# Optimization experiments

Measured on AMD Instinct MI355X. Metric: run time of the kernel, lower is better.

Reference implementation:

```python
import jax, jax.numpy as jnp
import numpy as np

IN_CH = 12      # InChannels global in original code
GROWTH = 12     # growth global == growthRate
H = 34          # peptide/pseudo-sequence length (long==34 branch)
BN_EPS = 1e-5


def setup_inputs() -> dict:
    key = jax.random.key(0)
    k = jax.random.split(key, 5)
    B, C = 16384, 72  # C = IN_CH + 5*GROWTH
    x = jax.random.normal(k[0], (B, C, H, 1), dtype=jnp.float32)
    gamma = jnp.ones((C,), dtype=jnp.float32)
    beta = jnp.zeros((C,), dtype=jnp.float32)
    conv_w = jax.random.normal(k[1], (GROWTH, C, 3, 1), dtype=jnp.float32) * 0.05
    fc_w = jax.random.normal(k[2], (1, H), dtype=jnp.float32)
    fc_bias = jax.random.normal(k[3], (1,), dtype=jnp.float32)
    return {"x": x, "gamma": gamma, "beta": beta, "conv_w": conv_w,
            "fc_w": fc_w, "fc_bias": fc_bias}


def reference(x, gamma, beta, conv_w, fc_w, fc_bias):
    B, C, Hh, Ww = x.shape
    n = (C - IN_CH) // GROWTH  # number of growth groups
    sg = jax.lax.stop_gradient

    x1 = x[:, :IN_CH]                                 # [B,12,H,1]
    x2g = x[:, IN_CH:].reshape(B, n, GROWTH, Hh, 1)    # [B,n,g,H,1]

    # per-group channel means, squeezed over the width-1 axis -> [B,n,H]
    m = x2g.mean(axis=2)[..., 0]
    x11 = x1.mean(axis=1)[..., 0]                      # [B,H]

    w = fc_w[0]                                        # [H]
    lin_m = m @ w + fc_bias[0]                         # [B,n]  (bias included per F.linear call)
    lin_out = lin_m[:, -1]                             # lin(x_outt), [B]
    lin_x11 = x11 @ w + fc_bias[0]                     # [B]

    # gate for x1: sigmoid(lin(x_outt) + lin(x11)); note bias appears twice, as in torch
    g1 = jax.nn.sigmoid(lin_out + lin_x11)             # [B]
    # gates for groups 0..n-2: sigmoid(lin(group_i) + lin(x_outt))
    gates = jax.nn.sigmoid(lin_m[:, :-1] + lin_out[:, None])  # [B,n-1]

    # the expand/repeat/view dance collapses to a per-sample scalar gate broadcast
    x1g = g1[:, None, None, None] * sg(x1)             # x1 is detached in original
    # groups are appended in reversed order (i = n-2 .. 0)
    gg = gates[:, ::-1][:, :, None, None, None] * sg(x2g[:, :-1][:, ::-1])
    gg_flat = gg.reshape(B, (n - 1) * GROWTH, Hh, 1)
    x_out = x2g[:, -1]                                 # last group, appended ungated

    xxx = jnp.concatenate([x1g, gg_flat, x_out], axis=1)  # [B,C,H,1]

    # BatchNorm2d in training mode (batch statistics, biased variance)
    mu = xxx.mean(axis=(0, 2, 3), keepdims=True)
    var = xxx.var(axis=(0, 2, 3), keepdims=True)
    xn = (xxx - mu) * jax.lax.rsqrt(var + BN_EPS)
    h = jax.nn.relu(gamma[None, :, None, None] * xn + beta[None, :, None, None])

    # Conv2d(C -> GROWTH, kernel (3,1), padding (1,0), no bias)
    out = jax.lax.conv_general_dilated(
        h, conv_w, window_strides=(1, 1), padding=((1, 1), (0, 0)),
        dimension_numbers=("NCHW", "OIHW", "NCHW"))

    return jnp.concatenate([x, out], axis=1)           # [B, C+GROWTH, H, 1]
```

## Files before the change

kernel.cpp:

```cpp
#include <hip/hip_runtime.h>
#include <math.h>


#define BN_EPS 1e-5f

#define WS_S    0
#define WS_SS   72
#define WS_A    144
#define WS_B    216
#define WS_WT   288
#define WS_GATE (288 + 3456)

__device__ __forceinline__ float sigmoidf_(float z) { return 1.f / (1.f + expf(-z)); }

__global__ __launch_bounds__(256) void k1_stats(const float* __restrict__ x,
                                                const float* __restrict__ fw,
                                                const float* __restrict__ fb,
                                                float* __restrict__ ws,
                                                int B, int nTrip)
{
    __shared__ float xs[3 * 2520];
    __shared__ float rs_s[3][72];
    __shared__ float rss_s[3][72];
    __shared__ float wsum_s[3][72];
    __shared__ float sc_s[3][8];
    __shared__ float Sacc[72], SSacc[72];

    const int tid = threadIdx.x;
    if (tid < 72) { Sacc[tid] = 0.f; SSacc[tid] = 0.f; }

    for (int t = blockIdx.x; t < nTrip; t += gridDim.x) {
        const int b0 = t * 3;

        for (int idx = tid; idx < 3 * 612; idx += 256) {
            int g = idx / 612, v = idx - g * 612;
            int b = b0 + g;
            if (b < B) {
                float4 q = ((const float4*)(x + (size_t)b * 2448))[v];
                float vv[4] = {q.x, q.y, q.z, q.w};
#pragma unroll
                for (int j = 0; j < 4; ++j) {
                    int e = v * 4 + j;
                    int c = e / 34, h = e - c * 34;
                    xs[g * 2520 + c * 35 + h] = vv[j];
                }
            }
        }
        __syncthreads();

        if (tid < 216) {
            int g = tid / 72, c = tid - g * 72;
            float rs = 0.f, rss = 0.f, wsm = 0.f;
            if (b0 + g < B) {
                const float* p = &xs[g * 2520 + c * 35];
#pragma unroll
                for (int h = 0; h < 34; ++h) {
                    float v = p[h];
                    rs += v;
                    rss = fmaf(v, v, rss);
                    wsm = fmaf(v, fw[h], wsm);
                }
            }
            rs_s[g][c] = rs; rss_s[g][c] = rss; wsum_s[g][c] = wsm;
        }
        __syncthreads();

        if (tid < 3 && b0 + tid < B) {
            int g = tid;
            float lm[6];
#pragma unroll
            for (int r = 0; r < 6; ++r) {
                float s = 0.f;
                for (int c = 0; c < 12; ++c) s += wsum_s[g][r * 12 + c];
                lm[r] = s * (1.f / 12.f) + fb[0];
            }
            float lin_out = lm[5];
            float sc[6];
            sc[0] = sigmoidf_(lin_out + lm[0]);
            sc[1] = sigmoidf_(lm[4] + lin_out);
            sc[2] = sigmoidf_(lm[3] + lin_out);
            sc[3] = sigmoidf_(lm[2] + lin_out);
            sc[4] = sigmoidf_(lm[1] + lin_out);
            sc[5] = 1.f;
            float* gb = ws + WS_GATE + (size_t)(b0 + g) * 6;
#pragma unroll
            for (int r = 0; r < 6; ++r) { sc_s[g][r] = sc[r]; gb[r] = sc[r]; }
        }
        __syncthreads();

        if (tid < 72) {
            const int c = tid;
            const int r = c / 12;
            const int dd[6] = {0, 36, 12, -12, -36, 0};
            const int src = c + dd[r];
            float a = 0.f, q = 0.f;
#pragma unroll
            for (int g = 0; g < 3; ++g) {
                if (b0 + g < B) {
                    float s = sc_s[g][r];
                    a = fmaf(s, rs_s[g][src], a);
                    q = fmaf(s * s, rss_s[g][src], q);
                }
            }
            Sacc[c] += a; SSacc[c] += q;
        }
        __syncthreads();
    }

    if (tid < 72) {
        atomicAdd(&ws[WS_S + tid], Sacc[tid]);
        atomicAdd(&ws[WS_SS + tid], SSacc[tid]);
    }
}

__global__ void k2_finalize(const float* __restrict__ gamma,
                            const float* __restrict__ beta,
                            const float* __restrict__ cw,
                            float* __restrict__ ws, float invN)
{
    const int tid = threadIdx.x;
    if (tid < 72) {
        float S = ws[WS_S + tid], SS = ws[WS_SS + tid];
        float mu = S * invN;
        float var = SS * invN - mu * mu;
        float inv = rsqrtf(var + BN_EPS);
        float A = gamma[tid] * inv;
        ws[WS_A + tid] = A;
        ws[WS_B + tid] = beta[tid] - mu * A;
    }
    for (int i = tid; i < 12 * 72 * 3; i += 256) {
        int o = i / 216, rem = i - o * 216;
        int c = rem / 3, k = rem - c * 3;
        ws[WS_WT + c * 48 + o * 4 + k] = cw[i];
    }
}

__global__ __launch_bounds__(256) void k3_out(const float* __restrict__ x,
                                              const float* __restrict__ ws,
                                              float* __restrict__ out, int B)
{
    __shared__ float hp[6 * 2592];
    __shared__ float2 AB[72];
    __shared__ float gl[6][8];

    const int tid = threadIdx.x;
    const int b0 = blockIdx.x * 6;
    int nb = B - b0; if (nb > 6) nb = 6;

    if (tid < 72) AB[tid] = make_float2(ws[WS_A + tid], ws[WS_B + tid]);
    for (int t2 = tid; t2 < nb * 6; t2 += 256) {
        int g = t2 / 6, j = t2 - g * 6;
        gl[g][j] = ws[WS_GATE + (size_t)(b0 + g) * 6 + j];
    }
    for (int t2 = tid; t2 < nb * 72; t2 += 256) {
        int g = t2 / 72, c = t2 - g * 72;
        hp[g * 2592 + c * 36] = 0.f;
        hp[g * 2592 + c * 36 + 35] = 0.f;
    }
    __syncthreads();

    for (int idx = tid; idx < nb * 612; idx += 256) {
        int g = idx / 612, v = idx - g * 612;
        size_t b = (size_t)(b0 + g);
        float4 q = ((const float4*)(x + b * 2448))[v];
        ((float4*)(out + b * 2856))[v] = q;
        float vv[4] = {q.x, q.y, q.z, q.w};
#pragma unroll
        for (int j = 0; j < 4; ++j) {
            int e = v * 4 + j;
            int cx = e / 34, h = e - cx * 34;
            const int ddv[6]  = {0, 36, 12, -12, -36, 0};
            const int sidx[6] = {0, 4, 3, 2, 1, 5};
            int rx = cx / 12;
            int cdst = cx + ddv[rx];
            float2 ab = AB[cdst];
            float s = gl[g][sidx[rx]];
            hp[g * 2592 + cdst * 36 + h + 1] = fmaxf(fmaf(ab.x * s, vv[j], ab.y), 0.f);
        }
    }
    __syncthreads();

    const float4* wT = (const float4*)(ws + WS_WT);
    for (int it = tid; it < nb * 34; it += 256) {
        int g = it / 34, hh = it - g * 34;
        const float* hb = &hp[g * 2592];
        float acc[12];
#pragma unroll
        for (int o = 0; o < 12; ++o) acc[o] = 0.f;
        for (int c = 0; c < 72; ++c) {
            float h0 = hb[c * 36 + hh];
            float h1 = hb[c * 36 + hh + 1];
            float h2 = hb[c * 36 + hh + 2];
#pragma unroll
            for (int o = 0; o < 12; ++o) {
                float4 wv = wT[c * 12 + o];
                acc[o] = fmaf(h0, wv.x, fmaf(h1, wv.y, fmaf(h2, wv.z, acc[o])));
            }
        }
        float* op = out + (size_t)(b0 + g) * 2856 + 2448;
#pragma unroll
        for (int o = 0; o < 12; ++o) op[o * 34 + hh] = acc[o];
    }
}

extern "C" void kernel_launch(void* const* d_in, const int* in_sizes, int n_in,
                              void* d_out, int out_size, void* d_ws, size_t ws_size,
                              hipStream_t stream)
{
    const float* x     = (const float*)d_in[0];
    const float* gamma = (const float*)d_in[1];
    const float* beta  = (const float*)d_in[2];
    const float* cw    = (const float*)d_in[3];
    const float* fw    = (const float*)d_in[4];
    const float* fb    = (const float*)d_in[5];
    float* out = (float*)d_out;
    float* ws  = (float*)d_ws;

    const int B = in_sizes[0] / (72 * 34);
    const int nTrip = (B + 2) / 3;

    hipMemsetAsync(ws, 0, 144 * sizeof(float), stream);

    k1_stats<<<1024, 256, 0, stream>>>(x, fw, fb, ws, B, nTrip);
    k2_finalize<<<1, 256, 0, stream>>>(gamma, beta, cw, ws, 1.f / ((float)B * 34.f));
    const int nb3 = (B + 5) / 6;
    k3_out<<<nb3, 256, 0, stream>>>(x, ws, out, B);
}
```

Measured before the change: 470.0 us.

## Read stats directly from global, store activations in fp16 LDS, deterministic partial reduce

```diff
diff --git a/kernel.cpp b/kernel.cpp
--- a/kernel.cpp
+++ b/kernel.cpp
@@ -1,4 +1,5 @@
 #include <hip/hip_runtime.h>
+#include <hip/hip_fp16.h>
 #include <math.h>
 
 
@@ -9,7 +10,8 @@
 #define WS_A    144
 #define WS_B    216
 #define WS_WT   288
-#define WS_GATE (288 + 3456)
+#define WS_GATE 3744
+#define K1_BLOCKS 512
 
 __device__ __forceinline__ float sigmoidf_(float z) { return 1.f / (1.f + expf(-z)); }
 
@@ -17,106 +19,100 @@
                                                 const float* __restrict__ fw,
                                                 const float* __restrict__ fb,
                                                 float* __restrict__ ws,
+                                                float* __restrict__ part,
                                                 int B, int nTrip)
 {
-    __shared__ float xs[3 * 2520];
-    __shared__ float rs_s[3][72];
-    __shared__ float rss_s[3][72];
-    __shared__ float wsum_s[3][72];
+    __shared__ float rs_s[3][72], rss_s[3][72], wsum_s[3][72];
+    __shared__ float lm_s[3][6];
     __shared__ float sc_s[3][8];
-    __shared__ float Sacc[72], SSacc[72];
+    __shared__ float Sacc[144];
 
     const int tid = threadIdx.x;
-    if (tid < 72) { Sacc[tid] = 0.f; SSacc[tid] = 0.f; }
-
-    for (int t = blockIdx.x; t < nTrip; t += gridDim.x) {
+    const int g = tid / 72;
+    const int c = tid - g * 72;
+    if (tid < 144) Sacc[tid] = 0.f;
+
+    for (int t = blockIdx.x; t < nTrip; t += K1_BLOCKS) {
         const int b0 = t * 3;
 
-        for (int idx = tid; idx < 3 * 612; idx += 256) {
-            int g = idx / 612, v = idx - g * 612;
-            int b = b0 + g;
-            if (b < B) {
-                float4 q = ((const float4*)(x + (size_t)b * 2448))[v];
-                float vv[4] = {q.x, q.y, q.z, q.w};
-#pragma unroll
-                for (int j = 0; j < 4; ++j) {
-                    int e = v * 4 + j;
-                    int c = e / 34, h = e - c * 34;
-                    xs[g * 2520 + c * 35 + h] = vv[j];
+        if (tid < 216 && b0 + g < B) {
+            const float2* p = (const float2*)(x + (size_t)(b0 + g) * 2448 + c * 34);
+            float rs = 0.f, rss = 0.f, wsm = 0.f;
+#pragma unroll
+            for (int i = 0; i < 17; ++i) {
+                float2 v = p[i];
+                rs += v.x + v.y;
+                rss = fmaf(v.x, v.x, fmaf(v.y, v.y, rss));
+                wsm = fmaf(v.x, fw[2 * i], fmaf(v.y, fw[2 * i + 1], wsm));
+            }
+            rs_s[g][c] = rs; rss_s[g][c] = rss; wsum_s[g][c] = wsm;
+        }
+        __syncthreads();
+
+        if (tid < 18) {
+            int gg = tid / 6, r = tid - gg * 6;
+            float s = 0.f;
+#pragma unroll
+            for (int k = 0; k < 12; ++k) s += wsum_s[gg][r * 12 + k];
+            lm_s[gg][r] = s * (1.f / 12.f) + fb[0];
+        }
+        __syncthreads();
+
+        if (tid < 3 && b0 + tid < B) {
+            float lin_out = lm_s[tid][5];
+            float sc[6];
+            sc[0] = sigmoidf_(lin_out + lm_s[tid][0]);
+            sc[1] = sigmoidf_(lm_s[tid][4] + lin_out);
+            sc[2] = sigmoidf_(lm_s[tid][3] + lin_out);
+            sc[3] = sigmoidf_(lm_s[tid][2] + lin_out);
+            sc[4] = sigmoidf_(lm_s[tid][1] + lin_out);
+            sc[5] = 1.f;
+            float* gb = ws + WS_GATE + (size_t)(b0 + tid) * 6;
+#pragma unroll
+            for (int r = 0; r < 6; ++r) { sc_s[tid][r] = sc[r]; gb[r] = sc[r]; }
+        }
+        __syncthreads();
+
+        if (tid < 72) {
+            const int r = tid / 12;
+            const int dd[6] = {0, 36, 12, -12, -36, 0};
+            const int src = tid + dd[r];
+            float a = 0.f, q = 0.f;
+#pragma unroll
+            for (int gg = 0; gg < 3; ++gg) {
+                if (b0 + gg < B) {
+                    float s = sc_s[gg][r];
+                    a = fmaf(s, rs_s[gg][src], a);
+                    q = fmaf(s * s, rss_s[gg][src], q);
                 }
             }
-        }
-        __syncthreads();
-
-        if (tid < 216) {
-            int g = tid / 72, c = tid - g * 72;
-            float rs = 0.f, rss = 0.f, wsm = 0.f;
-            if (b0 + g < B) {
-                const float* p = &xs[g * 2520 + c * 35];
-#pragma unroll
-                for (int h = 0; h < 34; ++h) {
-                    float v = p[h];
-                    rs += v;
-                    rss = fmaf(v, v, rss);
-                    wsm = fmaf(v, fw[h], wsm);
-                }
-            }
-            rs_s[g][c] = rs; rss_s[g][c] = rss; wsum_s[g][c] = wsm;
-        }
-        __syncthreads();
-
-        if (tid < 3 && b0 + tid < B) {
-            int g = tid;
-            float lm[6];
-#pragma unroll
-            for (int r = 0; r < 6; ++r) {
-                float s = 0.f;
-                for (int c = 0; c < 12; ++c) s += wsum_s[g][r * 12 + c];
-                lm[r] = s * (1.f / 12.f) + fb[0];
-            }
-            float lin_out = lm[5];
-            float sc[6];
-            sc[0] = sigmoidf_(lin_out + lm[0]);
-            sc[1] = sigmoidf_(lm[4] + lin_out);
-            sc[2] = sigmoidf_(lm[3] + lin_out);
-            sc[3] = sigmoidf_(lm[2] + lin_out);
-            sc[4] = sigmoidf_(lm[1] + lin_out);
-            sc[5] = 1.f;
-            float* gb = ws + WS_GATE + (size_t)(b0 + g) * 6;
-#pragma unroll
-            for (int r = 0; r < 6; ++r) { sc_s[g][r] = sc[r]; gb[r] = sc[r]; }
-        }
-        __syncthreads();
-
-        if (tid < 72) {
-            const int c = tid;
-            const int r = c / 12;
-            const int dd[6] = {0, 36, 12, -12, -36, 0};
-            const int src = c + dd[r];
-            float a = 0.f, q = 0.f;
-#pragma unroll
-            for (int g = 0; g < 3; ++g) {
-                if (b0 + g < B) {
-                    float s = sc_s[g][r];
-                    a = fmaf(s, rs_s[g][src], a);
-                    q = fmaf(s * s, rss_s[g][src], q);
-                }
-            }
-            Sacc[c] += a; SSacc[c] += q;
-        }
-        __syncthreads();
-    }
-
-    if (tid < 72) {
-        atomicAdd(&ws[WS_S + tid], Sacc[tid]);
-        atomicAdd(&ws[WS_SS + tid], SSacc[tid]);
-    }
-}
-
-__global__ void k2_finalize(const float* __restrict__ gamma,
-                            const float* __restrict__ beta,
-                            const float* __restrict__ cw,
-                            float* __restrict__ ws, float invN)
+            Sacc[tid] += a; Sacc[72 + tid] += q;
+        }
+        __syncthreads();
+    }
+
+    if (tid < 144) part[(size_t)tid * K1_BLOCKS + blockIdx.x] = Sacc[tid];
+}
+
+__global__ __launch_bounds__(256) void k2a_reduce(float* __restrict__ ws,
+                                                  const float* __restrict__ part)
+{
+    const int ch = blockIdx.x;
+    const float* p = part + (size_t)ch * K1_BLOCKS;
+    float s = 0.f;
+    for (int i = threadIdx.x; i < K1_BLOCKS; i += 256) s += p[i];
+#pragma unroll
+    for (int off = 32; off; off >>= 1) s += __shfl_down(s, off, 64);
+    __shared__ float wsum[4];
+    if ((threadIdx.x & 63) == 0) wsum[threadIdx.x >> 6] = s;
+    __syncthreads();
+    if (threadIdx.x == 0) ws[WS_S + ch] = wsum[0] + wsum[1] + wsum[2] + wsum[3];
+}
+
+__global__ void k2b_finalize(const float* __restrict__ gamma,
+                             const float* __restrict__ beta,
+                             const float* __restrict__ cw,
+                             float* __restrict__ ws, float invN)
 {
     const int tid = threadIdx.x;
     if (tid < 72) {
@@ -139,58 +135,72 @@
                                               const float* __restrict__ ws,
                                               float* __restrict__ out, int B)
 {
-    __shared__ float hp[6 * 2592];
-    __shared__ float2 AB[72];
+    __shared__ __align__(16) __half hs[6 * 2456];
+    __shared__ float2 AB[73];
     __shared__ float gl[6][8];
 
     const int tid = threadIdx.x;
     const int b0 = blockIdx.x * 6;
     int nb = B - b0; if (nb > 6) nb = 6;
 
-    if (tid < 72) AB[tid] = make_float2(ws[WS_A + tid], ws[WS_B + tid]);
+    if (tid < 73)
+        AB[tid] = (tid < 72) ? make_float2(ws[WS_A + tid], ws[WS_B + tid])
+                             : make_float2(0.f, 0.f);
     for (int t2 = tid; t2 < nb * 6; t2 += 256) {
         int g = t2 / 6, j = t2 - g * 6;
         gl[g][j] = ws[WS_GATE + (size_t)(b0 + g) * 6 + j];
     }
-    for (int t2 = tid; t2 < nb * 72; t2 += 256) {
-        int g = t2 / 72, c = t2 - g * 72;
-        hp[g * 2592 + c * 36] = 0.f;
-        hp[g * 2592 + c * 36 + 35] = 0.f;
+    if (tid < 24) {
+        int g = tid >> 2, k = tid & 3;
+        ((unsigned int*)hs)[g * 1228 + ((k < 2) ? k : (1224 + k))] = 0u;
     }
     __syncthreads();
 
     for (int idx = tid; idx < nb * 612; idx += 256) {
-        int g = idx / 612, v = idx - g * 612;
+        int g = idx / 612, v4 = idx - g * 612;
         size_t b = (size_t)(b0 + g);
-        float4 q = ((const float4*)(x + b * 2448))[v];
-        ((float4*)(out + b * 2856))[v] = q;
+        float4 q = ((const float4*)(x + b * 2448))[v4];
+        ((float4*)(out + b * 2856))[v4] = q;
+
+        const int ddc[6]  = {0, 36, 12, -12, -36, 0};
+        const int sidx[6] = {0, 4, 3, 2, 1, 5};
+        int rx = v4 / 102;
+        int e  = v4 * 4;
+        int cx0 = e / 34;
+        int h0i = e - cx0 * 34;
+        int dd  = ddc[rx];
+        int cd0 = cx0 + dd;
+        float2 ab0 = AB[cd0];
+        float2 ab1 = AB[cd0 + 1];
+        float s = gl[g][sidx[rx]];
         float vv[4] = {q.x, q.y, q.z, q.w};
+        __half hv[4];
 #pragma unroll
         for (int j = 0; j < 4; ++j) {
-            int e = v * 4 + j;
-            int cx = e / 34, h = e - cx * 34;
-            const int ddv[6]  = {0, 36, 12, -12, -36, 0};
-            const int sidx[6] = {0, 4, 3, 2, 1, 5};
-            int rx = cx / 12;
-            int cdst = cx + ddv[rx];
-            float2 ab = AB[cdst];
-            float s = gl[g][sidx[rx]];
-            hp[g * 2592 + cdst * 36 + h + 1] = fmaxf(fmaf(ab.x * s, vv[j], ab.y), 0.f);
-        }
+            float2 ab = (h0i + j >= 34) ? ab1 : ab0;
+            hv[j] = __float2half(fmaxf(fmaf(ab.x * s, vv[j], ab.y), 0.f));
+        }
+        union { __half2 h2; unsigned int u; } pa, pb;
+        pa.h2 = __halves2half2(hv[0], hv[1]);
+        pb.h2 = __halves2half2(hv[2], hv[3]);
+        int dst = g * 2456 + 4 + e + dd * 34;
+        *reinterpret_cast<uint2*>(&hs[dst]) = make_uint2(pa.u, pb.u);
     }
     __syncthreads();
 
     const float4* wT = (const float4*)(ws + WS_WT);
     for (int it = tid; it < nb * 34; it += 256) {
         int g = it / 34, hh = it - g * 34;
-        const float* hb = &hp[g * 2592];
+        const __half* hb = &hs[g * 2456 + 4 + hh];
+        float m0 = (hh == 0) ? 0.f : 1.f;
+        float m2 = (hh == 33) ? 0.f : 1.f;
         float acc[12];
 #pragma unroll
         for (int o = 0; o < 12; ++o) acc[o] = 0.f;
         for (int c = 0; c < 72; ++c) {
-            float h0 = hb[c * 36 + hh];
-            float h1 = hb[c * 36 + hh + 1];
-            float h2 = hb[c * 36 + hh + 2];
+            float h0 = m0 * __half2float(hb[c * 34 - 1]);
+            float h1 =      __half2float(hb[c * 34]);
+            float h2 = m2 * __half2float(hb[c * 34 + 1]);
 #pragma unroll
             for (int o = 0; o < 12; ++o) {
                 float4 wv = wT[c * 12 + o];
@@ -218,11 +228,10 @@
 
     const int B = in_sizes[0] / (72 * 34);
     const int nTrip = (B + 2) / 3;
-
-    hipMemsetAsync(ws, 0, 144 * sizeof(float), stream);
-
-    k1_stats<<<1024, 256, 0, stream>>>(x, fw, fb, ws, B, nTrip);
-    k2_finalize<<<1, 256, 0, stream>>>(gamma, beta, cw, ws, 1.f / ((float)B * 34.f));
-    const int nb3 = (B + 5) / 6;
-    k3_out<<<nb3, 256, 0, stream>>>(x, ws, out, B);
-}
+    float* part = ws + WS_GATE + (size_t)B * 6;
+
+    k1_stats<<<K1_BLOCKS, 256, 0, stream>>>(x, fw, fb, ws, part, B, nTrip);
+    k2a_reduce<<<144, 256, 0, stream>>>(ws, part);
+    k2b_finalize<<<1, 256, 0, stream>>>(gamma, beta, cw, ws, 1.f / ((float)B * 34.f));
+    k3_out<<<(B + 5) / 6, 256, 0, stream>>>(x, ws, out, B);
+}
```

Measured after the change: 402.8 us. 1.17x faster.
